# Kernel optimization log

Hardware: AMD Instinct MI355X
Metric: run time of the kernel (lower is better)

The kernel has to match this reference:

```python
import jax, jax.numpy as jnp
import numpy as np

D_MODEL = 1024
N_HEADS = 16
HEAD_DIM = D_MODEL // N_HEADS
BATCH = 2
SEQ = 2048


def setup_inputs() -> dict:
    key = jax.random.key(0)
    ks = jax.random.split(key, 9)
    s = 1.0 / np.sqrt(D_MODEL)
    inp = {
        "x": jax.random.normal(ks[0], (BATCH, SEQ, D_MODEL), dtype=jnp.float32),
        "Wq": jax.random.uniform(ks[1], (D_MODEL, D_MODEL), jnp.float32, -s, s),
        "bq": jax.random.uniform(ks[2], (D_MODEL,), jnp.float32, -s, s),
        "Wk": jax.random.uniform(ks[3], (D_MODEL, D_MODEL), jnp.float32, -s, s),
        "bk": jax.random.uniform(ks[4], (D_MODEL,), jnp.float32, -s, s),
        "Wv": jax.random.uniform(ks[5], (D_MODEL, D_MODEL), jnp.float32, -s, s),
        "bv": jax.random.uniform(ks[6], (D_MODEL,), jnp.float32, -s, s),
        "Wo": jax.random.uniform(ks[7], (D_MODEL, D_MODEL), jnp.float32, -s, s),
        "bo": jax.random.uniform(ks[8], (D_MODEL,), jnp.float32, -s, s),
    }
    return inp


def reference(x, Wq, bq, Wk, bk, Wv, bv, Wo, bo):
    B, S, _ = x.shape
    # projections -> [B, H, S, Dh]
    def proj(W, b):
        y = jnp.einsum('bsd,df->bsf', x, W) + b
        return y.reshape(B, S, N_HEADS, HEAD_DIM).transpose(0, 2, 1, 3)
    q = proj(Wq, bq)
    k = proj(Wk, bk)
    v = proj(Wv, bv)
    scores = jnp.einsum('bhqd,bhkd->bhqk', q, k) / jnp.sqrt(jnp.float32(HEAD_DIM))
    mask = jnp.tril(jnp.ones((S, S), dtype=bool))  # [S, S] causal mask
    scores = jnp.where(mask, scores, -jnp.inf)
    weights = jax.nn.softmax(scores, axis=-1)
    h = jnp.einsum('bhqk,bhkd->bhqd', weights, v)
    h = h.transpose(0, 2, 1, 3).reshape(B, S, N_HEADS * HEAD_DIM)
    return jnp.einsum('bsd,df->bsf', h, Wo) + bo
```

## Files before the change

### kernel.cpp

```cpp
#include <hip/hip_runtime.h>
#include <hip/hip_bf16.h>
#include <cmath>

#define D_MODEL 1024
#define NHEADS 16
#define HDIM 64
#define BATCH 2
#define SEQ 2048
#define MROWS (BATCH*SEQ)
#define KDIM 1024

typedef unsigned short ushort_t;
typedef unsigned int uint32;
typedef __attribute__((ext_vector_type(8))) short short8;
typedef __attribute__((ext_vector_type(4))) float floatx4;

#define QSCALE 0.1803368801111204f
#define EXP2F(x) __builtin_amdgcn_exp2f(x)

__device__ __forceinline__ ushort_t f2bf(float x) {
    union { float f; uint32 u; } v; v.f = x;
    uint32 r = v.u + 0x7FFFu + ((v.u >> 16) & 1u);
    return (ushort_t)(r >> 16);
}

__device__ __forceinline__ uint32 pkbf(float a, float b) {
    union { __hip_bfloat162 h2; uint32 u; } v;
    v.h2 = __float22bfloat162_rn(make_float2(a, b));
    return v.u;
}

__device__ __forceinline__ void glds16(const void* g, void* l) {
    __builtin_amdgcn_global_load_lds(
        (const __attribute__((address_space(1))) void*)g,
        (__attribute__((address_space(3))) void*)l, 16, 0, 0);
}

__global__ __launch_bounds__(256)
void cvt_all(const float* __restrict__ x, const float* __restrict__ W0,
             const float* __restrict__ W1, const float* __restrict__ W2,
             const float* __restrict__ W3, ushort_t* __restrict__ xb,
             ushort_t* __restrict__ WtQKV, ushort_t* __restrict__ WtO)
{
    const int z = blockIdx.z;
    if (z == 4) {
        size_t idx = ((size_t)blockIdx.y * 32 + blockIdx.x) * 256 + threadIdx.x;
        #pragma unroll
        for (int l = 0; l < 4; ++l) {
            size_t i = ((size_t)l * 262144 + idx) * 4;
            float4 v = *(const float4*)(x + i);
            uint2 o;
            o.x = pkbf(v.x, v.y);
            o.y = pkbf(v.z, v.w);
            *(uint2*)(xb + i) = o;
        }
        return;
    }
    __shared__ float tl[32][33];
    const float* W = (z == 0) ? W0 : (z == 1) ? W1 : (z == 2) ? W2 : W3;
    ushort_t* out = (z < 3) ? (WtQKV + (size_t)z * D_MODEL * KDIM) : WtO;
    const int k0 = blockIdx.x * 32, n0 = blockIdx.y * 32;
    const int tx = threadIdx.x & 31, ty = threadIdx.x >> 5;
    #pragma unroll
    for (int i = 0; i < 4; ++i)
        tl[ty + i * 8][tx] = W[(size_t)(k0 + ty + i * 8) * D_MODEL + n0 + tx];
    __syncthreads();
    #pragma unroll
    for (int i = 0; i < 4; ++i)
        out[(size_t)(n0 + ty + i * 8) * KDIM + k0 + tx] = f2bf(tl[tx][ty + i * 8]);
}

template<int BN>
__global__ __launch_bounds__(256)
void gemm_mfma(const ushort_t* __restrict__ A, const ushort_t* __restrict__ Bt,
               const float* __restrict__ b0, const float* __restrict__ b1,
               const float* __restrict__ b2, float* __restrict__ Cf,
               ushort_t* __restrict__ Qb, ushort_t* __restrict__ Kb,
               ushort_t* __restrict__ Vb, int mode)
{
    constexpr int NT = BN / 32;
    constexpr int BC = BN / 32;
    __shared__ ushort_t As[128 * 64];
    __shared__ ushort_t Bs[BN * 64];

    const int tid = threadIdx.x;
    const int w = tid >> 6, lane = tid & 63;
    const int quad = lane >> 4, col = lane & 15;
    const int m0 = blockIdx.y * 128, n0 = blockIdx.x * BN;
    const int mbase = (w & 1) * 64, nbase = (w >> 1) * (BN / 2);

    floatx4 zero = {0.f, 0.f, 0.f, 0.f};
    floatx4 acc[4][NT];
    #pragma unroll
    for (int i = 0; i < 4; ++i)
        #pragma unroll
        for (int j = 0; j < NT; ++j) acc[i][j] = zero;

    #pragma unroll 1
    for (int k0 = 0; k0 < KDIM; k0 += 64) {
        #pragma unroll
        for (int i = 0; i < 4; ++i) {
            int c = (w * 4 + i) * 64 + lane;
            int row = c >> 3;
            int kc = (c & 7) ^ (row & 7);
            glds16(A + (size_t)(m0 + row) * KDIM + k0 + kc * 8, As + (w * 4 + i) * 512);
        }
        #pragma unroll
        for (int i = 0; i < BC; ++i) {
            int c = (w * BC + i) * 64 + lane;
            int row = c >> 3;
            int kc = (c & 7) ^ (row & 7);
            glds16(Bt + (size_t)(n0 + row) * KDIM + k0 + kc * 8, Bs + (w * BC + i) * 512);
        }
        __syncthreads();
        #pragma unroll
        for (int ks = 0; ks < 2; ++ks) {
            short8 af[4], bfr[NT];
            const int kc = ks * 4 + quad;
            #pragma unroll
            for (int mt = 0; mt < 4; ++mt) {
                int r = mbase + mt * 16 + col;
                af[mt] = *(const short8*)(As + ((size_t)r * 8 + (kc ^ (r & 7))) * 8);
            }
            #pragma unroll
            for (int nt = 0; nt < NT; ++nt) {
                int r = nbase + nt * 16 + col;
                bfr[nt] = *(const short8*)(Bs + ((size_t)r * 8 + (kc ^ (r & 7))) * 8);
            }
            #pragma unroll
            for (int mt = 0; mt < 4; ++mt)
                #pragma unroll
                for (int nt = 0; nt < NT; ++nt)
                    acc[mt][nt] = __builtin_amdgcn_mfma_f32_16x16x32_bf16(
                        af[mt], bfr[nt], acc[mt][nt], 0, 0, 0);
        }
        __syncthreads();
    }

    if (mode == 0) {
        #pragma unroll
        for (int mt = 0; mt < 4; ++mt)
            #pragma unroll
            for (int nt = 0; nt < NT; ++nt) {
                int n = n0 + nbase + nt * 16 + col;
                float bb = b0[n];
                #pragma unroll
                for (int r = 0; r < 4; ++r) {
                    int m = m0 + mbase + mt * 16 + quad * 4 + r;
                    Cf[(size_t)m * D_MODEL + n] = acc[mt][nt][r] + bb;
                }
            }
    } else {
        const int which = n0 >> 10;
        const float* bp = (which == 0) ? b0 : (which == 1) ? b1 : b2;
        if (which < 2) {
            ushort_t* outp = (which == 0) ? Qb : Kb;
            const float scl = (which == 0) ? QSCALE : 1.0f;
            #pragma unroll
            for (int mt = 0; mt < 4; ++mt)
                #pragma unroll
                for (int nt = 0; nt < NT; ++nt) {
                    int nn = (n0 + nbase + nt * 16 + col) & 1023;
                    float bb = bp[nn];
                    int h = nn >> 6, d = nn & 63;
                    #pragma unroll
                    for (int r = 0; r < 4; ++r) {
                        int m = m0 + mbase + mt * 16 + quad * 4 + r;
                        int b = m >> 11, s = m & 2047;
                        outp[((size_t)(b * NHEADS + h) * SEQ + s) * HDIM + d] =
                            f2bf((acc[mt][nt][r] + bb) * scl);
                    }
                }
        } else {
            #pragma unroll
            for (int mt = 0; mt < 4; ++mt)
                #pragma unroll
                for (int nt = 0; nt < NT; ++nt) {
                    int nn = (n0 + nbase + nt * 16 + col) & 1023;
                    float bb = bp[nn];
                    int h = nn >> 6, d = nn & 63;
                    int mb = m0 + mbase + mt * 16 + quad * 4;
                    int b = mb >> 11, s = mb & 2047;
                    uint2 pw;
                    pw.x = pkbf(acc[mt][nt][0] + bb, acc[mt][nt][1] + bb);
                    pw.y = pkbf(acc[mt][nt][2] + bb, acc[mt][nt][3] + bb);
                    *(uint2*)(Vb + ((size_t)(b * NHEADS + h) * HDIM + d) * SEQ + s) = pw;
                }
        }
    }
}

__global__ __launch_bounds__(128)
void attn_mfma(const ushort_t* __restrict__ Q, const ushort_t* __restrict__ K,
               const ushort_t* __restrict__ Vt, ushort_t* __restrict__ H)
{
    __shared__ ushort_t Ks[64 * 64];
    __shared__ ushort_t Vs[64 * 64];
    __shared__ ushort_t Ps[32 * 64];

    const int tid = threadIdx.x;
    const int w = tid >> 6, lane = tid & 63;
    const int quad = lane >> 4, col = lane & 15;
    const int blk = blockIdx.x;
    const int bh = (blk & 7) * 4 + ((blk >> 3) & 3);
    const int pair = blk >> 5;
    const size_t base = (size_t)bh * SEQ * HDIM;
    const ushort_t* Kb = K + base;
    const ushort_t* Vb = Vt + base;
    const int b = bh >> 4, h = bh & 15;
    const int qrow = w * 16 + col;

    int srow[4], soff[4];
    #pragma unroll
    for (int i = 0; i < 4; ++i) {
        int c = i * 128 + tid;
        srow[i] = c >> 3;
        soff[i] = ((c & 7) ^ ((c >> 3) & 7)) * 8;
    }

    const floatx4 zero = {0.f, 0.f, 0.f, 0.f};

    #pragma unroll 1
    for (int pi = 0; pi < 2; ++pi) {
        const int qt = pi ? pair : 63 - pair;
        const int q0 = qt * 32;
        const int nt = (qt >> 1) + 1;

        short8 bq[2];
        bq[0] = *(const short8*)(Q + base + (size_t)(q0 + qrow) * HDIM + quad * 8);
        bq[1] = *(const short8*)(Q + base + (size_t)(q0 + qrow) * HDIM + 32 + quad * 8);

        floatx4 o[4];
        #pragma unroll
        for (int j = 0; j < 4; ++j) o[j] = zero;
        float mreg = -INFINITY, lreg = 0.f;

        #pragma unroll 1
        for (int t = 0; t < nt; ++t) {
            const int k0 = t * 64;
            __syncthreads();
            #pragma unroll
            for (int i = 0; i < 4; ++i) {
                const int cb = i * 128 + w * 64;
                glds16(Kb + (size_t)(k0 + srow[i]) * HDIM + soff[i], Ks + (size_t)cb * 8);
                glds16(Vb + (size_t)srow[i] * SEQ + k0 + soff[i],    Vs + (size_t)cb * 8);
            }
            __syncthreads();

            floatx4 sc[4];
            #pragma unroll
            for (int j = 0; j < 4; ++j) sc[j] = zero;
            #pragma unroll
            for (int ks = 0; ks < 2; ++ks) {
                const int kc = ks * 4 + quad;
                #pragma unroll
                for (int j = 0; j < 4; ++j) {
                    int rk = j * 16 + col;
                    short8 ak = *(const short8*)(Ks + ((size_t)rk * 8 + (kc ^ (rk & 7))) * 8);
                    sc[j] = __builtin_amdgcn_mfma_f32_16x16x32_bf16(ak, bq[ks], sc[j], 0, 0, 0);
                }
            }

            if (t == nt - 1) {
                const int qg = q0 + qrow - k0;
                #pragma unroll
                for (int j = 0; j < 4; ++j)
                    #pragma unroll
                    for (int r = 0; r < 4; ++r)
                        if (j * 16 + quad * 4 + r > qg) sc[j][r] = -INFINITY;
            }

            float mx = -INFINITY;
            #pragma unroll
            for (int j = 0; j < 4; ++j)
                mx = fmaxf(mx, fmaxf(fmaxf(sc[j][0], sc[j][1]), fmaxf(sc[j][2], sc[j][3])));
            mx = fmaxf(mx, __shfl_xor(mx, 16));
            mx = fmaxf(mx, __shfl_xor(mx, 32));
            float mn = fmaxf(mreg, mx);
            float alpha = EXP2F(mreg - mn);
            mreg = mn;

            float ls = 0.f;
            #pragma unroll
            for (int j = 0; j < 4; ++j) {
                float p0 = EXP2F(sc[j][0] - mn);
                float p1 = EXP2F(sc[j][1] - mn);
                float p2 = EXP2F(sc[j][2] - mn);
                float p3 = EXP2F(sc[j][3] - mn);
                ls += (p0 + p1) + (p2 + p3);
                uint2 pw;
                pw.x = pkbf(p0, p1);
                pw.y = pkbf(p2, p3);
                int c = 2 * j + (quad >> 1);
                *(uint2*)(Ps + ((size_t)qrow * 8 + (c ^ (qrow & 7))) * 8 + (quad & 1) * 4) = pw;
            }
            ls += __shfl_xor(ls, 16);
            ls += __shfl_xor(ls, 32);
            lreg = lreg * alpha + ls;
            #pragma unroll
            for (int j = 0; j < 4; ++j) {
                o[j][0] *= alpha; o[j][1] *= alpha; o[j][2] *= alpha; o[j][3] *= alpha;
            }

            #pragma unroll
            for (int ks = 0; ks < 2; ++ks) {
                const int kc = ks * 4 + quad;
                short8 bp = *(const short8*)(Ps + ((size_t)qrow * 8 + (kc ^ (qrow & 7))) * 8);
                #pragma unroll
                for (int j = 0; j < 4; ++j) {
                    int rv = j * 16 + col;
                    short8 av = *(const short8*)(Vs + ((size_t)rv * 8 + (kc ^ (rv & 7))) * 8);
                    o[j] = __builtin_amdgcn_mfma_f32_16x16x32_bf16(av, bp, o[j], 0, 0, 0);
                }
            }
        }

        const float linv = 1.f / lreg;
        const size_t rowb = ((size_t)(b * SEQ + q0 + qrow)) * D_MODEL + h * HDIM;
        #pragma unroll
        for (int j = 0; j < 4; ++j) {
            uint2 pw;
            pw.x = pkbf(o[j][0] * linv, o[j][1] * linv);
            pw.y = pkbf(o[j][2] * linv, o[j][3] * linv);
            *(uint2*)(H + rowb + j * 16 + quad * 4) = pw;
        }
    }
}

extern "C" void kernel_launch(void* const* d_in, const int* in_sizes, int n_in,
                              void* d_out, int out_size, void* d_ws, size_t ws_size,
                              hipStream_t stream)
{
    (void)in_sizes; (void)n_in; (void)out_size; (void)ws_size;
    const float* x  = (const float*)d_in[0];
    const float* Wq = (const float*)d_in[1];
    const float* bq = (const float*)d_in[2];
    const float* Wk = (const float*)d_in[3];
    const float* bk = (const float*)d_in[4];
    const float* Wv = (const float*)d_in[5];
    const float* bv = (const float*)d_in[6];
    const float* Wo = (const float*)d_in[7];
    const float* bo = (const float*)d_in[8];

    const size_t E = (size_t)MROWS * D_MODEL;
    ushort_t* xb    = (ushort_t*)d_ws;
    ushort_t* WtQKV = xb + E;
    ushort_t* WtO   = WtQKV + 3 * (size_t)D_MODEL * KDIM;
    ushort_t* Qb    = WtO + (size_t)D_MODEL * KDIM;
    ushort_t* Kb    = Qb + E;
    ushort_t* Vb    = Kb + E;
    ushort_t* Hb    = Vb + E;

    cvt_all<<<dim3(32, 32, 5), 256, 0, stream>>>(x, Wq, Wk, Wv, Wo, xb, WtQKV, WtO);
    gemm_mfma<128><<<dim3(24, 32), 256, 0, stream>>>(xb, WtQKV, bq, bk, bv,
                                                     nullptr, Qb, Kb, Vb, 1);
    attn_mfma<<<dim3(1024), 128, 0, stream>>>(Qb, Kb, Vb, Hb);
    gemm_mfma<64><<<dim3(16, 32), 256, 0, stream>>>(Hb, WtO, bo, nullptr, nullptr,
                                                    (float*)d_out, nullptr, nullptr, nullptr, 0);
}
```

Before: 211.5 us.

## Process 64-query tiles per block with two 16-row groups per wave

```diff
diff --git a/kernel.cpp b/kernel.cpp
--- a/kernel.cpp
+++ b/kernel.cpp
@@ -196,19 +196,21 @@
 {
     __shared__ ushort_t Ks[64 * 64];
     __shared__ ushort_t Vs[64 * 64];
-    __shared__ ushort_t Ps[32 * 64];
+    __shared__ ushort_t Ps[64 * 64];
 
     const int tid = threadIdx.x;
     const int w = tid >> 6, lane = tid & 63;
     const int quad = lane >> 4, col = lane & 15;
     const int blk = blockIdx.x;
     const int bh = (blk & 7) * 4 + ((blk >> 3) & 3);
-    const int pair = blk >> 5;
+    const int g = blk >> 5;
+    const int qt = (g < 8) ? 31 - g : (g < 16) ? g : (g < 24) ? 39 - g : g - 24;
+    const int q0 = qt * 64;
+    const int nt = qt + 1;
     const size_t base = (size_t)bh * SEQ * HDIM;
     const ushort_t* Kb = K + base;
     const ushort_t* Vb = Vt + base;
     const int b = bh >> 4, h = bh & 15;
-    const int qrow = w * 16 + col;
 
     int srow[4], soff[4];
     #pragma unroll
@@ -218,110 +220,129 @@
         soff[i] = ((c & 7) ^ ((c >> 3) & 7)) * 8;
     }
 
+    const int rq0 = w * 32 + col;
+    const int rq1 = w * 32 + 16 + col;
+    short8 bq[2][2];
+    #pragma unroll
+    for (int qg = 0; qg < 2; ++qg) {
+        const ushort_t* qp = Q + base + (size_t)(q0 + w * 32 + qg * 16 + col) * HDIM;
+        bq[0][qg] = *(const short8*)(qp + quad * 8);
+        bq[1][qg] = *(const short8*)(qp + 32 + quad * 8);
+    }
+
     const floatx4 zero = {0.f, 0.f, 0.f, 0.f};
+    floatx4 o[2][4];
+    #pragma unroll
+    for (int qg = 0; qg < 2; ++qg)
+        #pragma unroll
+        for (int j = 0; j < 4; ++j) o[qg][j] = zero;
+    float mreg[2] = {-INFINITY, -INFINITY};
+    float lreg[2] = {0.f, 0.f};
 
     #pragma unroll 1
-    for (int pi = 0; pi < 2; ++pi) {
-        const int qt = pi ? pair : 63 - pair;
-        const int q0 = qt * 32;
-        const int nt = (qt >> 1) + 1;
-
-        short8 bq[2];
-        bq[0] = *(const short8*)(Q + base + (size_t)(q0 + qrow) * HDIM + quad * 8);
-        bq[1] = *(const short8*)(Q + base + (size_t)(q0 + qrow) * HDIM + 32 + quad * 8);
-
-        floatx4 o[4];
-        #pragma unroll
-        for (int j = 0; j < 4; ++j) o[j] = zero;
-        float mreg = -INFINITY, lreg = 0.f;
-
-        #pragma unroll 1
-        for (int t = 0; t < nt; ++t) {
-            const int k0 = t * 64;
-            __syncthreads();
-            #pragma unroll
-            for (int i = 0; i < 4; ++i) {
-                const int cb = i * 128 + w * 64;
-                glds16(Kb + (size_t)(k0 + srow[i]) * HDIM + soff[i], Ks + (size_t)cb * 8);
-                glds16(Vb + (size_t)srow[i] * SEQ + k0 + soff[i],    Vs + (size_t)cb * 8);
-            }
-            __syncthreads();
-
-            floatx4 sc[4];
-            #pragma unroll
-            for (int j = 0; j < 4; ++j) sc[j] = zero;
-            #pragma unroll
-            for (int ks = 0; ks < 2; ++ks) {
-                const int kc = ks * 4 + quad;
-                #pragma unroll
-                for (int j = 0; j < 4; ++j) {
-                    int rk = j * 16 + col;
-                    short8 ak = *(const short8*)(Ks + ((size_t)rk * 8 + (kc ^ (rk & 7))) * 8);
-                    sc[j] = __builtin_amdgcn_mfma_f32_16x16x32_bf16(ak, bq[ks], sc[j], 0, 0, 0);
-                }
-            }
-
-            if (t == nt - 1) {
-                const int qg = q0 + qrow - k0;
+    for (int t = 0; t < nt; ++t) {
+        const int k0 = t * 64;
+        __syncthreads();
+        #pragma unroll
+        for (int i = 0; i < 4; ++i) {
+            const int cb = i * 128 + w * 64;
+            glds16(Kb + (size_t)(k0 + srow[i]) * HDIM + soff[i], Ks + (size_t)cb * 8);
+            glds16(Vb + (size_t)srow[i] * SEQ + k0 + soff[i],    Vs + (size_t)cb * 8);
+        }
+        __syncthreads();
+
+        floatx4 sc[2][4];
+        #pragma unroll
+        for (int qg = 0; qg < 2; ++qg)
+            #pragma unroll
+            for (int j = 0; j < 4; ++j) sc[qg][j] = zero;
+        #pragma unroll
+        for (int ks = 0; ks < 2; ++ks) {
+            const int kc = ks * 4 + quad;
+            #pragma unroll
+            for (int j = 0; j < 4; ++j) {
+                int rk = j * 16 + col;
+                short8 ak = *(const short8*)(Ks + ((size_t)rk * 8 + (kc ^ (rk & 7))) * 8);
+                sc[0][j] = __builtin_amdgcn_mfma_f32_16x16x32_bf16(ak, bq[ks][0], sc[0][j], 0, 0, 0);
+                sc[1][j] = __builtin_amdgcn_mfma_f32_16x16x32_bf16(ak, bq[ks][1], sc[1][j], 0, 0, 0);
+            }
+        }
+
+        if (t == nt - 1) {
+            #pragma unroll
+            for (int qg = 0; qg < 2; ++qg) {
+                const int qloc = w * 32 + qg * 16 + col;
                 #pragma unroll
                 for (int j = 0; j < 4; ++j)
                     #pragma unroll
                     for (int r = 0; r < 4; ++r)
-                        if (j * 16 + quad * 4 + r > qg) sc[j][r] = -INFINITY;
-            }
-
+                        if (j * 16 + quad * 4 + r > qloc) sc[qg][j][r] = -INFINITY;
+            }
+        }
+
+        #pragma unroll
+        for (int qg = 0; qg < 2; ++qg) {
+            const int rq = qg ? rq1 : rq0;
             float mx = -INFINITY;
             #pragma unroll
             for (int j = 0; j < 4; ++j)
-                mx = fmaxf(mx, fmaxf(fmaxf(sc[j][0], sc[j][1]), fmaxf(sc[j][2], sc[j][3])));
+                mx = fmaxf(mx, fmaxf(fmaxf(sc[qg][j][0], sc[qg][j][1]),
+                                     fmaxf(sc[qg][j][2], sc[qg][j][3])));
             mx = fmaxf(mx, __shfl_xor(mx, 16));
             mx = fmaxf(mx, __shfl_xor(mx, 32));
-            float mn = fmaxf(mreg, mx);
-            float alpha = EXP2F(mreg - mn);
-            mreg = mn;
+            float mn = fmaxf(mreg[qg], mx);
+            float alpha = EXP2F(mreg[qg] - mn);
+            mreg[qg] = mn;
 
             float ls = 0.f;
             #pragma unroll
             for (int j = 0; j < 4; ++j) {
-                float p0 = EXP2F(sc[j][0] - mn);
-                float p1 = EXP2F(sc[j][1] - mn);
-                float p2 = EXP2F(sc[j][2] - mn);
-                float p3 = EXP2F(sc[j][3] - mn);
+                float p0 = EXP2F(sc[qg][j][0] - mn);
+                float p1 = EXP2F(sc[qg][j][1] - mn);
+                float p2 = EXP2F(sc[qg][j][2] - mn);
+                float p3 = EXP2F(sc[qg][j][3] - mn);
                 ls += (p0 + p1) + (p2 + p3);
                 uint2 pw;
                 pw.x = pkbf(p0, p1);
                 pw.y = pkbf(p2, p3);
                 int c = 2 * j + (quad >> 1);
-                *(uint2*)(Ps + ((size_t)qrow * 8 + (c ^ (qrow & 7))) * 8 + (quad & 1) * 4) = pw;
+                *(uint2*)(Ps + ((size_t)rq * 8 + (c ^ (rq & 7))) * 8 + (quad & 1) * 4) = pw;
             }
             ls += __shfl_xor(ls, 16);
             ls += __shfl_xor(ls, 32);
-            lreg = lreg * alpha + ls;
+            lreg[qg] = lreg[qg] * alpha + ls;
             #pragma unroll
             for (int j = 0; j < 4; ++j) {
-                o[j][0] *= alpha; o[j][1] *= alpha; o[j][2] *= alpha; o[j][3] *= alpha;
-            }
-
-            #pragma unroll
-            for (int ks = 0; ks < 2; ++ks) {
-                const int kc = ks * 4 + quad;
-                short8 bp = *(const short8*)(Ps + ((size_t)qrow * 8 + (kc ^ (qrow & 7))) * 8);
-                #pragma unroll
-                for (int j = 0; j < 4; ++j) {
-                    int rv = j * 16 + col;
-                    short8 av = *(const short8*)(Vs + ((size_t)rv * 8 + (kc ^ (rv & 7))) * 8);
-                    o[j] = __builtin_amdgcn_mfma_f32_16x16x32_bf16(av, bp, o[j], 0, 0, 0);
-                }
-            }
-        }
-
-        const float linv = 1.f / lreg;
-        const size_t rowb = ((size_t)(b * SEQ + q0 + qrow)) * D_MODEL + h * HDIM;
+                o[qg][j][0] *= alpha; o[qg][j][1] *= alpha;
+                o[qg][j][2] *= alpha; o[qg][j][3] *= alpha;
+            }
+        }
+
+        #pragma unroll
+        for (int ks = 0; ks < 2; ++ks) {
+            const int kc = ks * 4 + quad;
+            short8 bp0 = *(const short8*)(Ps + ((size_t)rq0 * 8 + (kc ^ (rq0 & 7))) * 8);
+            short8 bp1 = *(const short8*)(Ps + ((size_t)rq1 * 8 + (kc ^ (rq1 & 7))) * 8);
+            #pragma unroll
+            for (int j = 0; j < 4; ++j) {
+                int rv = j * 16 + col;
+                short8 av = *(const short8*)(Vs + ((size_t)rv * 8 + (kc ^ (rv & 7))) * 8);
+                o[0][j] = __builtin_amdgcn_mfma_f32_16x16x32_bf16(av, bp0, o[0][j], 0, 0, 0);
+                o[1][j] = __builtin_amdgcn_mfma_f32_16x16x32_bf16(av, bp1, o[1][j], 0, 0, 0);
+            }
+        }
+    }
+
+    #pragma unroll
+    for (int qg = 0; qg < 2; ++qg) {
+        const float linv = 1.f / lreg[qg];
+        const int s = q0 + w * 32 + qg * 16 + col;
+        const size_t rowb = ((size_t)(b * SEQ + s)) * D_MODEL + h * HDIM;
         #pragma unroll
         for (int j = 0; j < 4; ++j) {
             uint2 pw;
-            pw.x = pkbf(o[j][0] * linv, o[j][1] * linv);
-            pw.y = pkbf(o[j][2] * linv, o[j][3] * linv);
+            pw.x = pkbf(o[qg][j][0] * linv, o[qg][j][1] * linv);
+            pw.y = pkbf(o[qg][j][2] * linv, o[qg][j][3] * linv);
             *(uint2*)(H + rowb + j * 16 + quad * 4) = pw;
         }
     }
```

Result: no change. 210.5 us (-0.5%).
